# Optimization experiments

Hardware: AMD Instinct MI355X
Metric: run time of the kernel (lower is better)

The kernel has to match this reference:

```python
import jax, jax.numpy as jnp
import numpy as np

DIM = 1024
HIDDEN = 2560  # multiple_of*(int(2*4*DIM/3)//multiple_of)
N_EXPERTS = 4
TOP_K = 2


def setup_inputs() -> dict:
    key = jax.random.key(0)
    ks = jax.random.split(key, 5)
    scale_d = 1.0 / np.sqrt(DIM)
    scale_h = 1.0 / np.sqrt(HIDDEN)
    x = jax.random.normal(ks[0], (8, 1024, DIM), dtype=jnp.float32)
    gate_w = jax.random.normal(ks[1], (N_EXPERTS, DIM), dtype=jnp.float32) * scale_d
    # torch Linear weight layout [out, in]; stacked over experts
    w1 = jax.random.normal(ks[2], (N_EXPERTS, HIDDEN, DIM), dtype=jnp.float32) * scale_d
    w3 = jax.random.normal(ks[3], (N_EXPERTS, HIDDEN, DIM), dtype=jnp.float32) * scale_d
    w2 = jax.random.normal(ks[4], (N_EXPERTS, DIM, HIDDEN), dtype=jnp.float32) * scale_h
    return {"x": x, "gate_w": gate_w, "w1": w1, "w2": w2, "w3": w3}


def reference(x, gate_w, w1, w2, w3):
    orig_shape = x.shape
    xf = x.reshape(-1, orig_shape[-1])  # [N, D]

    # gating: softmax -> top-k -> renormalize
    logits = jnp.einsum('nd,ed->ne', xf, gate_w)
    probs = jax.nn.softmax(logits, axis=-1)
    topk_w, topk_idx = jax.lax.top_k(probs, TOP_K)          # [N, K]
    topk_w = topk_w / jnp.sum(topk_w, axis=-1, keepdims=True)

    # per-token per-expert combine weight (0 if expert not selected)
    one_hot = jax.nn.one_hot(topk_idx, N_EXPERTS, dtype=xf.dtype)  # [N, K, E]
    comb = jnp.einsum('nk,nke->ne', topk_w, one_hot)               # [N, E]

    # dense per-expert SwiGLU FFN (4 experts), then weighted combine
    h1 = jnp.einsum('nd,ehd->neh', xf, w1)   # [N, E, H]
    h3 = jnp.einsum('nd,ehd->neh', xf, w3)
    h = jax.nn.silu(h1) * h3
    y = jnp.einsum('neh,edh->ned', h, w2)    # [N, E, D]
    out = jnp.einsum('ned,ne->nd', y, comb)  # [N, D]

    aux_loss = jnp.asarray(0.0, dtype=x.dtype)  # eval mode
    return out.reshape(orig_shape), aux_loss
```

## Files before the change

kernel.cpp:

```cpp
#include <hip/hip_runtime.h>

typedef unsigned short u16;
typedef unsigned int   u32;

#define DIM  1024
#define HID  2560
#define NTOK 8192
#define NEXP 4

#define BM 128
#define BN 128
#define BK 64

#define ESEG 4352
#define NROWS (NEXP * ESEG)

typedef __attribute__((ext_vector_type(8))) short bf16x8;
typedef __attribute__((ext_vector_type(4))) float f32x4;

__device__ __forceinline__ void async16(const void* g, void* l) {
  __builtin_amdgcn_global_load_lds((const __attribute__((address_space(1))) u32*)g,
                                   (__attribute__((address_space(3))) u32*)l,
                                   16, 0, 0);
}
__device__ __forceinline__ u16 f2bf(float f) {
  union { float f; u32 u; } c; c.f = f;
  u32 u = c.u;
  return (u16)((u + 0x7fffu + ((u >> 16) & 1u)) >> 16);
}
__device__ __forceinline__ ushort4 cvt4(float4 v) {
  ushort4 o; o.x = f2bf(v.x); o.y = f2bf(v.y); o.z = f2bf(v.z); o.w = f2bf(v.w);
  return o;
}

__global__ void zrt_kernel(int* __restrict__ rt) {
  if (threadIdx.x < 8) rt[threadIdx.x] = 0;
}

__global__ void cvt13_kernel(const float* __restrict__ w1, const float* __restrict__ w3,
                             u16* __restrict__ w1b, u16* __restrict__ w3b, int n4each) {
  int i = blockIdx.x * blockDim.x + threadIdx.x;
  if (i < n4each)
    ((ushort4*)w1b)[i] = cvt4(((const float4*)w1)[i]);
  else if (i < 2 * n4each)
    ((ushort4*)w3b)[i - n4each] = cvt4(((const float4*)w3)[i - n4each]);
}

__global__ void cvt2_kernel(const float* __restrict__ w2, u16* __restrict__ w2b, int n4) {
  int i = blockIdx.x * blockDim.x + threadIdx.x;
  if (i < n4) ((ushort4*)w2b)[i] = cvt4(((const float4*)w2)[i]);
}

__global__ void gate_kernel(const float* __restrict__ X, const float* __restrict__ GW,
                            float* __restrict__ comb, int* __restrict__ rt,
                            u16* __restrict__ Xb, int* __restrict__ idxpool,
                            float* __restrict__ out, int out_n) {
  __shared__ int s_pick[8];

  int gtid = blockIdx.x * blockDim.x + threadIdx.x;

  {
    int n4 = out_n >> 2;
    int stride = gridDim.x * blockDim.x;
    float4 z = {0.f, 0.f, 0.f, 0.f};
    for (int j = gtid; j < n4; j += stride) ((float4*)out)[j] = z;
    if (gtid == 0)
      for (int j = n4 << 2; j < out_n; ++j) out[j] = 0.f;
  }

  int tok  = gtid >> 6;
  int lane = gtid & 63;
  int widx = threadIdx.x >> 6;

  const float4* xv = (const float4*)(X + (size_t)tok * DIM + lane * 16);
  float4 x0 = xv[0], x1 = xv[1], x2 = xv[2], x3 = xv[3];

  ushort4* xb = (ushort4*)(Xb + (size_t)tok * DIM + lane * 16);
  xb[0] = cvt4(x0); xb[1] = cvt4(x1); xb[2] = cvt4(x2); xb[3] = cvt4(x3);

  float acc[NEXP];
#pragma unroll
  for (int e = 0; e < NEXP; ++e) {
    const float4* gv = (const float4*)(GW + e * DIM + lane * 16);
    float4 g0 = gv[0], g1 = gv[1], g2 = gv[2], g3 = gv[3];
    float s;
    s  = x0.x * g0.x + x0.y * g0.y + x0.z * g0.z + x0.w * g0.w;
    s += x1.x * g1.x + x1.y * g1.y + x1.z * g1.z + x1.w * g1.w;
    s += x2.x * g2.x + x2.y * g2.y + x2.z * g2.z + x2.w * g2.w;
    s += x3.x * g3.x + x3.y * g3.y + x3.z * g3.z + x3.w * g3.w;
    acc[e] = s;
  }
#pragma unroll
  for (int off = 32; off > 0; off >>= 1) {
#pragma unroll
    for (int e = 0; e < NEXP; ++e) acc[e] += __shfl_xor(acc[e], off);
  }
  if (lane == 0) {
    int i1 = 0;
#pragma unroll
    for (int e = 1; e < NEXP; ++e) if (acc[e] > acc[i1]) i1 = e;
    int i2 = -1;
#pragma unroll
    for (int e = 0; e < NEXP; ++e) {
      if (e == i1) continue;
      if (i2 < 0 || acc[e] > acc[i2]) i2 = e;
    }
    float m  = acc[i1];
    float e1 = __expf(acc[i1] - m), e2 = __expf(acc[i2] - m);
    float inv = 1.f / (e1 + e2);
    float w[NEXP] = {0.f, 0.f, 0.f, 0.f};
    w[i1] = e1 * inv; w[i2] = e2 * inv;
#pragma unroll
    for (int e = 0; e < NEXP; ++e) comb[(size_t)tok * NEXP + e] = w[e];
    s_pick[2 * widx]     = i1;
    s_pick[2 * widx + 1] = i2;
  }
  __syncthreads();

  if (threadIdx.x < 64) {
    int tid0 = threadIdx.x;
    int p  = (tid0 < 8) ? s_pick[tid0] : -1;
    int tk = blockIdx.x * 4 + (tid0 >> 1);
#pragma unroll
    for (int e = 0; e < NEXP; ++e) {
      unsigned long long b = __ballot(p == e);
      int cw = __popcll(b);
      if (cw) {
        int src = __ffsll((unsigned long long)b) - 1;
        int bp = 0;
        if (tid0 == src) bp = atomicAdd(&rt[4 + e], cw);
        bp = __shfl(bp, src);
        if (p == e) {
          int off = __popcll(b & ((1ull << tid0) - 1ull));
          int slot = bp + off;
          if (slot < ESEG) idxpool[e * ESEG + slot] = tk;
        }
      }
    }
  }
}


__global__ __launch_bounds__(256, 2) void ffn13_kernel(
    const u16* __restrict__ Xb, const u16* __restrict__ W1,
    const u16* __restrict__ W3, const float* __restrict__ combp,
    const int* __restrict__ idxpool, const int* __restrict__ rt,
    u16* __restrict__ Hpool) {
  const int e   = blockIdx.y >> 6;
  const int mb  = blockIdx.y & 63;
  int cnt = rt[4 + e]; if (cnt > ESEG) cnt = ESEG;
  const int m0  = mb * BM;
  if (m0 >= cnt) return;
  const int rbase = e * ESEG;
  const int n0    = blockIdx.x * BN;

  __shared__ __align__(16) u16 As [BM * BK];
  __shared__ __align__(16) u16 B1s[BN * BK];
  __shared__ __align__(16) u16 B3s[BN * BK];
  __shared__ float s_comb[BM];
  __shared__ int   s_idx [BM];

  const int tid  = threadIdx.x;
  const int wave = tid >> 6;
  const int lane = tid & 63;

  if (tid < BM) {
    int m = m0 + tid;
    int t = (m < cnt) ? idxpool[rbase + m] : 0;
    s_idx[tid]  = t;
    s_comb[tid] = combp[(size_t)t * NEXP + e];
  }
  __syncthreads();

  const u16* W1e = W1 + (size_t)e * HID * DIM;
  const u16* W3e = W3 + (size_t)e * HID * DIM;

  const int scc = (((tid & 7) ^ ((tid >> 3) & 7)) << 3);
  const int r0  = tid >> 3;
  const u16 *pA[4], *pB1[4], *pB3[4];
  int dsto[4];
#pragma unroll
  for (int q = 0; q < 4; ++q) {
    int row = r0 + 32 * q;
    pA[q]   = Xb  + (size_t)s_idx[row] * DIM + scc;
    pB1[q]  = W1e + (size_t)(n0 + row) * DIM + scc;
    pB3[q]  = W3e + (size_t)(n0 + row) * DIM + scc;
    dsto[q] = (tid + 256 * q) * 8;
  }

  const int wm = (wave >> 1) * 64, wn = (wave & 1) * 64;
  const int quad = lane >> 4, r = lane & 15;

  f32x4 acc1[4][4], acc3[4][4];
#pragma unroll
  for (int i = 0; i < 4; ++i)
#pragma unroll
    for (int j = 0; j < 4; ++j) {
      acc1[i][j] = (f32x4){0.f, 0.f, 0.f, 0.f};
      acc3[i][j] = (f32x4){0.f, 0.f, 0.f, 0.f};
    }

  for (int k0 = 0; k0 < DIM; k0 += BK) {
    __syncthreads();
#pragma unroll
    for (int q = 0; q < 4; ++q) { async16(pA[q],  &As [dsto[q]]); pA[q]  += BK; }
#pragma unroll
    for (int q = 0; q < 4; ++q) { async16(pB1[q], &B1s[dsto[q]]); pB1[q] += BK; }
#pragma unroll
    for (int q = 0; q < 4; ++q) { async16(pB3[q], &B3s[dsto[q]]); pB3[q] += BK; }
    __syncthreads();

#pragma unroll
    for (int s = 0; s < 2; ++s) {
      bf16x8 af[4], b1f[4], b3f[4];
#pragma unroll
      for (int i = 0; i < 4; ++i) {
        int row = wm + i * 16 + r;
        af[i] = *(const bf16x8*)&As[row * BK + ((((s << 2) + quad) ^ (row & 7)) << 3)];
      }
#pragma unroll
      for (int j = 0; j < 4; ++j) {
        int row = wn + j * 16 + r;
        int cc  = (((s << 2) + quad) ^ (row & 7)) << 3;
        b1f[j] = *(const bf16x8*)&B1s[row * BK + cc];
        b3f[j] = *(const bf16x8*)&B3s[row * BK + cc];
      }
#pragma unroll
      for (int i = 0; i < 4; ++i)
#pragma unroll
        for (int j = 0; j < 4; ++j) {
          acc1[i][j] = __builtin_amdgcn_mfma_f32_16x16x32_bf16(af[i], b1f[j], acc1[i][j], 0, 0, 0);
          acc3[i][j] = __builtin_amdgcn_mfma_f32_16x16x32_bf16(af[i], b3f[j], acc3[i][j], 0, 0, 0);
        }
    }
  }

#pragma unroll
  for (int i = 0; i < 4; ++i) {
    const int rowb = wm + i * 16 + quad * 4;
#pragma unroll
    for (int rr = 0; rr < 4; ++rr) {
      const float cw = s_comb[rowb + rr];
      u16* orow = Hpool + (size_t)(rbase + m0 + rowb + rr) * HID + n0 + wn + r;
#pragma unroll
      for (int j = 0; j < 4; ++j) {
        float v1v = acc1[i][j][rr];
        float v3v = acc3[i][j][rr];
        float sig = 1.f / (1.f + __expf(-v1v));
        orow[j * 16] = f2bf(cw * (v1v * sig * v3v));
      }
    }
  }
}

__global__ __launch_bounds__(256, 2) void ffn2_kernel(
    const u16* __restrict__ Hpool, const u16* __restrict__ W2b,
    const int* __restrict__ idxpool, const int* __restrict__ rt,
    float* __restrict__ Out) {
  __shared__ __align__(16) u16 As[2][BM * BK];
  __shared__ __align__(16) u16 Bs[2][BN * BK];
  __shared__ int s_idx[BM];

  const int x   = blockIdx.x & 7;
  const int e   = x >> 1;
  const int nbh = (x & 1) << 2;
  int cnt = rt[4 + e]; if (cnt > ESEG) cnt = ESEG;
  if (cnt == 0) return;
  const int Mb     = (cnt + BM - 1) >> 7;
  const int rbase  = e * ESEG;
  const int ntiles = Mb << 2;

  const int tid  = threadIdx.x;
  const int wave = tid >> 6;
  const int lane = tid & 63;
  const int scc  = (((tid & 7) ^ ((tid >> 3) & 7)) << 3);
  const int r0   = tid >> 3;
  const int wm = (wave >> 1) * 64, wn = (wave & 1) * 64;
  const int quad = lane >> 4, r = lane & 15;

  for (int t = blockIdx.x >> 3; t < ntiles; t += (gridDim.x >> 3)) {
    const int mb = t >> 2;
    const int nb = nbh + (t & 3);
    const int m0 = mb * BM;
    const int n0 = nb * BN;

    __syncthreads();
    if (tid < BM) {
      int m = m0 + tid;
      s_idx[tid] = (m < cnt) ? idxpool[rbase + m] : -1;
    }

    const u16 *pa[4], *pb[4];
    int dsto[4];
#pragma unroll
    for (int q = 0; q < 4; ++q) {
      int row = r0 + 32 * q;
      pa[q]   = Hpool + (size_t)(rbase + m0 + row) * HID + scc;
      pb[q]   = W2b + ((size_t)e * DIM + n0 + row) * HID + scc;
      dsto[q] = (tid + 256 * q) * 8;
    }

    f32x4 acc[4][4];
#pragma unroll
    for (int i = 0; i < 4; ++i)
#pragma unroll
      for (int j = 0; j < 4; ++j) acc[i][j] = (f32x4){0.f, 0.f, 0.f, 0.f};

#pragma unroll
    for (int q = 0; q < 4; ++q) { async16(pa[q], &As[0][dsto[q]]); pa[q] += BK; }
#pragma unroll
    for (int q = 0; q < 4; ++q) { async16(pb[q], &Bs[0][dsto[q]]); pb[q] += BK; }

    int cur = 0;
    const int NK = HID / BK;
    for (int k = 0; k < NK; ++k) {
      __syncthreads();

      if (k + 1 < NK) {
#pragma unroll
        for (int q = 0; q < 4; ++q) { async16(pa[q], &As[cur ^ 1][dsto[q]]); pa[q] += BK; }
#pragma unroll
        for (int q = 0; q < 4; ++q) { async16(pb[q], &Bs[cur ^ 1][dsto[q]]); pb[q] += BK; }
      }

#pragma unroll
      for (int s = 0; s < 2; ++s) {
        bf16x8 af[4], bf[4];
#pragma unroll
        for (int i = 0; i < 4; ++i) {
          int row = wm + i * 16 + r;
          af[i] = *(const bf16x8*)&As[cur][row * BK + ((((s << 2) + quad) ^ (row & 7)) << 3)];
        }
#pragma unroll
        for (int j = 0; j < 4; ++j) {
          int row = wn + j * 16 + r;
          bf[j] = *(const bf16x8*)&Bs[cur][row * BK + ((((s << 2) + quad) ^ (row & 7)) << 3)];
        }
#pragma unroll
        for (int i = 0; i < 4; ++i)
#pragma unroll
          for (int j = 0; j < 4; ++j)
            acc[i][j] = __builtin_amdgcn_mfma_f32_16x16x32_bf16(af[i], bf[j], acc[i][j], 0, 0, 0);
      }
      cur ^= 1;
    }

#pragma unroll
    for (int i = 0; i < 4; ++i) {
      const int rowb = wm + i * 16 + quad * 4;
#pragma unroll
      for (int rr = 0; rr < 4; ++rr) {
        int tk = s_idx[rowb + rr];
        if (tk >= 0) {
          float* orow = Out + (size_t)tk * DIM + n0 + wn + r;
#pragma unroll
          for (int j = 0; j < 4; ++j) unsafeAtomicAdd(&orow[j * 16], acc[i][j][rr]);
        }
      }
    }
  }
}

__global__ void ws_marker_kernel(float* __restrict__ Out, float v) {
  if (threadIdx.x == 0 && blockIdx.x == 0) Out[0] = v;
}

extern "C" void kernel_launch(void* const* d_in, const int* in_sizes, int n_in,
                              void* d_out, int out_size, void* d_ws, size_t ws_size,
                              hipStream_t stream) {
  const float* x  = (const float*)d_in[0];
  const float* gw = (const float*)d_in[1];
  const float* w1 = (const float*)d_in[2];
  const float* w2 = (const float*)d_in[3];
  const float* w3 = (const float*)d_in[4];
  float* out = (float*)d_out;

  const size_t WELEMS = (size_t)NEXP * HID * DIM;
  const size_t WBYTES = WELEMS * sizeof(u16);
  char* ws = (char*)d_ws;
  float* comb    = (float*)ws;
  int*   rt      = (int*)(ws + 131072);
  int*   idxpool = (int*)(ws + 131072 + 128);
  u16*   w1b     = (u16*)(ws + 131072 + 128 + (size_t)NROWS * 4);
  u16*   w2b     = w1b;
  u16*   w3b     = w1b + WELEMS;
  u16*   Xb      = w3b + WELEMS;
  u16*   Hpool   = Xb + (size_t)NTOK * DIM;

  const size_t need = 131072 + 128 + (size_t)NROWS * 4 + 2 * WBYTES +
                      (size_t)NTOK * DIM * sizeof(u16) +
                      (size_t)NROWS * HID * sizeof(u16);
  if (ws_size < need) {
    float v = 5000.0f + (float)((ws_size >> 20) > 999 ? 999 : (ws_size >> 20));
    ws_marker_kernel<<<dim3(1), dim3(64), 0, stream>>>(out, v);
    return;
  }

  zrt_kernel<<<dim3(1), dim3(64), 0, stream>>>(rt);

  gate_kernel<<<dim3(NTOK / 4), dim3(256), 0, stream>>>(x, gw, comb, rt, Xb,
                                                        idxpool, out, out_size / 4);

  {
    int n4each = (int)(WELEMS / 4);
    cvt13_kernel<<<dim3((2 * n4each + 255) / 256), dim3(256), 0, stream>>>(
        w1, w3, w1b, w3b, n4each);
  }

  ffn13_kernel<<<dim3(HID / BN, 64 * NEXP), dim3(256), 0, stream>>>(
      Xb, w1b, w3b, comb, idxpool, rt, Hpool);

  {
    int n4 = (int)(WELEMS / 4);
    cvt2_kernel<<<dim3((n4 + 255) / 256), dim3(256), 0, stream>>>(w2, w2b, n4);
  }

  ffn2_kernel<<<dim3(2048), dim3(256), 0, stream>>>(Hpool, w2b, idxpool, rt, out);
}
```

Before: 619.8 us.

## Rework ffn2 GEMM: smaller K tile, finer waitcnt pipelining, flat tile scheduling

Halves the ffn2 K tile to 32 so shared memory per block drops and occupancy can rise to 4 blocks per CU. It replaces the full syncthreads with explicit vmcnt waits plus barriers so the prefetch of the next stage overlaps the current MFMA work. It also swaps the fixed 8-way expert/column-half block assignment for a flat tile index over all experts, which balances work when expert counts are uneven. The risks are twice as many barrier steps per K pass, and hand-written waitcnt counts that must match the exact number of outstanding loads.

```diff
diff --git a/kernel.cpp b/kernel.cpp
--- a/kernel.cpp
+++ b/kernel.cpp
@@ -11,6 +11,7 @@
 #define BM 128
 #define BN 128
 #define BK 64
+#define BK2 32
 
 #define ESEG 4352
 #define NROWS (NEXP * ESEG)
@@ -140,7 +141,6 @@
   }
 }
 
-
 __global__ __launch_bounds__(256, 2) void ffn13_kernel(
     const u16* __restrict__ Xb, const u16* __restrict__ W1,
     const u16* __restrict__ W3, const float* __restrict__ combp,
@@ -253,34 +253,41 @@
   }
 }
 
-__global__ __launch_bounds__(256, 2) void ffn2_kernel(
+__global__ __launch_bounds__(256, 4) void ffn2_kernel(
     const u16* __restrict__ Hpool, const u16* __restrict__ W2b,
     const int* __restrict__ idxpool, const int* __restrict__ rt,
     float* __restrict__ Out) {
-  __shared__ __align__(16) u16 As[2][BM * BK];
-  __shared__ __align__(16) u16 Bs[2][BN * BK];
+  __shared__ __align__(16) u16 As[2][BM * BK2];
+  __shared__ __align__(16) u16 Bs[2][BN * BK2];
   __shared__ int s_idx[BM];
 
-  const int x   = blockIdx.x & 7;
-  const int e   = x >> 1;
-  const int nbh = (x & 1) << 2;
-  int cnt = rt[4 + e]; if (cnt > ESEG) cnt = ESEG;
-  if (cnt == 0) return;
-  const int Mb     = (cnt + BM - 1) >> 7;
-  const int rbase  = e * ESEG;
-  const int ntiles = Mb << 2;
+  int c0 = rt[4]; if (c0 > ESEG) c0 = ESEG;
+  int c1 = rt[5]; if (c1 > ESEG) c1 = ESEG;
+  int c2 = rt[6]; if (c2 > ESEG) c2 = ESEG;
+  int c3 = rt[7]; if (c3 > ESEG) c3 = ESEG;
+  const int M0 = (c0 + BM - 1) >> 7, M1 = (c1 + BM - 1) >> 7;
+  const int M2 = (c2 + BM - 1) >> 7, M3 = (c3 + BM - 1) >> 7;
+  const int b1 = M0 * 8, b2 = b1 + M1 * 8, b3 = b2 + M2 * 8;
+  const int total = b3 + M3 * 8;
 
   const int tid  = threadIdx.x;
   const int wave = tid >> 6;
   const int lane = tid & 63;
-  const int scc  = (((tid & 7) ^ ((tid >> 3) & 7)) << 3);
-  const int r0   = tid >> 3;
   const int wm = (wave >> 1) * 64, wn = (wave & 1) * 64;
   const int quad = lane >> 4, r = lane & 15;
 
-  for (int t = blockIdx.x >> 3; t < ntiles; t += (gridDim.x >> 3)) {
-    const int mb = t >> 2;
-    const int nb = nbh + (t & 3);
+  const int r0 = tid >> 2;
+  const int cc0 = tid & 3;
+
+  for (int t = blockIdx.x; t < total; t += gridDim.x) {
+    int e, tl, cnt, Mb;
+    if (t >= b3)      { e = 3; tl = t - b3; cnt = c3; Mb = M3; }
+    else if (t >= b2) { e = 2; tl = t - b2; cnt = c2; Mb = M2; }
+    else if (t >= b1) { e = 1; tl = t - b1; cnt = c1; Mb = M1; }
+    else              { e = 0; tl = t;      cnt = c0; Mb = M0; }
+    const int rbase = e * ESEG;
+    const int mb = tl % Mb;
+    const int nb = tl / Mb;
     const int m0 = mb * BM;
     const int n0 = nb * BN;
 
@@ -290,14 +297,15 @@
       s_idx[tid] = (m < cnt) ? idxpool[rbase + m] : -1;
     }
 
-    const u16 *pa[4], *pb[4];
-    int dsto[4];
-#pragma unroll
-    for (int q = 0; q < 4; ++q) {
-      int row = r0 + 32 * q;
-      pa[q]   = Hpool + (size_t)(rbase + m0 + row) * HID + scc;
-      pb[q]   = W2b + ((size_t)e * DIM + n0 + row) * HID + scc;
-      dsto[q] = (tid + 256 * q) * 8;
+    const u16 *pa[2], *pb[2];
+    int dst[2];
+#pragma unroll
+    for (int q = 0; q < 2; ++q) {
+      int row = r0 + 64 * q;
+      int scc = ((cc0 ^ ((row >> 1) & 3)) << 3);
+      pa[q]  = Hpool + (size_t)(rbase + m0 + row) * HID + scc;
+      pb[q]  = W2b + ((size_t)e * DIM + n0 + row) * HID + scc;
+      dst[q] = (tid + 256 * q) * 8;
     }
 
     f32x4 acc[4][4];
@@ -307,41 +315,44 @@
       for (int j = 0; j < 4; ++j) acc[i][j] = (f32x4){0.f, 0.f, 0.f, 0.f};
 
 #pragma unroll
-    for (int q = 0; q < 4; ++q) { async16(pa[q], &As[0][dsto[q]]); pa[q] += BK; }
-#pragma unroll
-    for (int q = 0; q < 4; ++q) { async16(pb[q], &Bs[0][dsto[q]]); pb[q] += BK; }
+    for (int q = 0; q < 2; ++q) { async16(pa[q], &As[0][dst[q]]); pa[q] += BK2; }
+#pragma unroll
+    for (int q = 0; q < 2; ++q) { async16(pb[q], &Bs[0][dst[q]]); pb[q] += BK2; }
 
     int cur = 0;
-    const int NK = HID / BK;
+    const int NK = HID / BK2;
     for (int k = 0; k < NK; ++k) {
-      __syncthreads();
-
       if (k + 1 < NK) {
 #pragma unroll
-        for (int q = 0; q < 4; ++q) { async16(pa[q], &As[cur ^ 1][dsto[q]]); pa[q] += BK; }
-#pragma unroll
-        for (int q = 0; q < 4; ++q) { async16(pb[q], &Bs[cur ^ 1][dsto[q]]); pb[q] += BK; }
-      }
-
-#pragma unroll
-      for (int s = 0; s < 2; ++s) {
-        bf16x8 af[4], bf[4];
-#pragma unroll
-        for (int i = 0; i < 4; ++i) {
-          int row = wm + i * 16 + r;
-          af[i] = *(const bf16x8*)&As[cur][row * BK + ((((s << 2) + quad) ^ (row & 7)) << 3)];
-        }
-#pragma unroll
-        for (int j = 0; j < 4; ++j) {
-          int row = wn + j * 16 + r;
-          bf[j] = *(const bf16x8*)&Bs[cur][row * BK + ((((s << 2) + quad) ^ (row & 7)) << 3)];
-        }
-#pragma unroll
-        for (int i = 0; i < 4; ++i)
-#pragma unroll
-          for (int j = 0; j < 4; ++j)
-            acc[i][j] = __builtin_amdgcn_mfma_f32_16x16x32_bf16(af[i], bf[j], acc[i][j], 0, 0, 0);
-      }
+        for (int q = 0; q < 2; ++q) { async16(pa[q], &As[cur ^ 1][dst[q]]); pa[q] += BK2; }
+#pragma unroll
+        for (int q = 0; q < 2; ++q) { async16(pb[q], &Bs[cur ^ 1][dst[q]]); pb[q] += BK2; }
+        asm volatile("s_waitcnt vmcnt(4)" ::: "memory");
+      } else {
+        asm volatile("s_waitcnt vmcnt(0)" ::: "memory");
+      }
+      __builtin_amdgcn_s_barrier();
+      asm volatile("" ::: "memory");
+
+      bf16x8 af[4], bf[4];
+#pragma unroll
+      for (int i = 0; i < 4; ++i) {
+        int row = wm + i * 16 + r;
+        af[i] = *(const bf16x8*)&As[cur][row * BK2 + ((quad ^ ((row >> 1) & 3)) << 3)];
+      }
+#pragma unroll
+      for (int j = 0; j < 4; ++j) {
+        int row = wn + j * 16 + r;
+        bf[j] = *(const bf16x8*)&Bs[cur][row * BK2 + ((quad ^ ((row >> 1) & 3)) << 3)];
+      }
+#pragma unroll
+      for (int i = 0; i < 4; ++i)
+#pragma unroll
+        for (int j = 0; j < 4; ++j)
+          acc[i][j] = __builtin_amdgcn_mfma_f32_16x16x32_bf16(af[i], bf[j], acc[i][j], 0, 0, 0);
+
+      asm volatile("" ::: "memory");
+      __builtin_amdgcn_s_barrier();
       cur ^= 1;
     }
 
```

New measurement: 615.9 us. About the same (-0.6%).
